# Kernel optimization log

Measured on AMD Instinct MI355X. Metric: run time of the kernel, lower is better.

Reference implementation:

```python
import jax, jax.numpy as jnp
import numpy as np

MIN_NORM = 1e-15
BALL_EPS = 4e-3  # HGCN PoincareBall fp32 boundary eps
C = 1.0          # curvature (init kwarg c)
CLAMP = 1e6      # torch.clamp bound in HypAgg.forward


def _artanh(x):
    # torch Artanh clamps input into open (-1, 1); use fp32-safe eps
    return jnp.arctanh(jnp.clip(x, -1.0 + 1e-7, 1.0 - 1e-7))


def _norm(x):
    return jnp.maximum(jnp.linalg.norm(x, axis=-1, keepdims=True), MIN_NORM)


def mobius_add(x, y, c):
    x2 = jnp.sum(x * x, axis=-1, keepdims=True)
    y2 = jnp.sum(y * y, axis=-1, keepdims=True)
    xy = jnp.sum(x * y, axis=-1, keepdims=True)
    num = (1.0 + 2.0 * c * xy + c * y2) * x + (1.0 - c * x2) * y
    den = 1.0 + 2.0 * c * xy + (c * c) * x2 * y2
    return num / jnp.maximum(den, MIN_NORM)


def lambda_x(x, c):
    return 2.0 / jnp.maximum(1.0 - c * jnp.sum(x * x, axis=-1, keepdims=True), MIN_NORM)


def logmap(p1, p2, c):
    # log_{p1}(p2) on the Poincare ball
    sub = mobius_add(-p1, p2, c)
    sub_norm = _norm(sub)
    sqrt_c = c ** 0.5
    return (2.0 / sqrt_c / lambda_x(p1, c)) * _artanh(sqrt_c * sub_norm) * sub / sub_norm


def expmap(u, p, c):
    sqrt_c = c ** 0.5
    u_norm = _norm(u)
    second = jnp.tanh(sqrt_c / 2.0 * lambda_x(p, c) * u_norm) * u / (sqrt_c * u_norm)
    return mobius_add(p, second, c)


def proj(x, c):
    norm = _norm(x)
    maxnorm = (1.0 - BALL_EPS) / (c ** 0.5)
    return jnp.where(norm > maxnorm, x / norm * maxnorm, x)


def setup_inputs() -> dict:
    key = jax.random.key(0)
    kx, ka, kw = jax.random.split(key, 3)
    B, N, D = 2, 768, 64
    # points strictly inside the unit ball
    x = proj(0.2 * jax.random.normal(kx, (B, N, D), dtype=jnp.float32), C)
    adj = (jax.random.uniform(ka, (B, N, N), dtype=jnp.float32) < 0.05).astype(jnp.float32)
    att_W = jax.random.normal(kw, (2 * D, 1), dtype=jnp.float32) * (1.0 / np.sqrt(2 * D))
    att_b = jnp.zeros((1,), dtype=jnp.float32)
    return {"x": x, "adj": adj, "att_W": att_W, "att_b": att_b}


def reference(x, adj, att_W, att_b):
    c = C
    b, n, d = x.shape
    # pairwise tangent vectors: x_local[b,i,j] = log_{x_i}(x_j)   (b,n,n,d)
    x_i = x[:, :, None, :]
    x_j = x[:, None, :, :]
    x_local = logmap(x_i, x_j, c)
    # log_x(x) == 0 tangent, kept for faithfulness
    x_self = logmap(x, x, c)  # (b,n,d), ~0
    # DenseAtt: linear(2d->1) on [self_tangent || pairwise_tangent], sigmoid, masked by adj
    feats = jnp.concatenate(
        [jnp.broadcast_to(x_self[:, :, None, :], x_local.shape), x_local], axis=-1
    )  # (b,n,n,2d)
    logits = jnp.einsum('bijk,ko->bijo', feats, att_W)[..., 0] + att_b[0]  # (b,n,n)
    att = jax.nn.sigmoid(logits) * adj
    # attention-weighted tangent aggregation over neighbors j
    support_t = jnp.einsum('bij,bijd->bid', att, x_local)
    # proj_tan is identity on the Poincare ball
    support_t = jnp.clip(support_t, -CLAMP, CLAMP)
    return proj(expmap(support_t, x, c), c)
```

## Files before the change

### kernel.cpp

```cpp
#include <hip/hip_runtime.h>
#include <math.h>

#define NB 2
#define NN 768
#define ND 64
#define XSTRIDE 68

__device__ __forceinline__ float fmul_(float a, float b) { float r = a * b; asm volatile("" : "+v"(r)); return r; }
__device__ __forceinline__ float fadd_(float a, float b) { float r = a + b; asm volatile("" : "+v"(r)); return r; }

template <typename F>
__device__ __forceinline__ float pw64(F f) {
  float r[8];
#pragma unroll
  for (int m = 0; m < 8; ++m) r[m] = f(m);
#pragma unroll
  for (int i = 1; i < 8; ++i) {
#pragma unroll
    for (int m = 0; m < 8; ++m) r[m] = fadd_(r[m], f(8 * i + m));
  }
  const float s01 = fadd_(r[0], r[1]), s23 = fadd_(r[2], r[3]);
  const float s45 = fadd_(r[4], r[5]), s67 = fadd_(r[6], r[7]);
  return fadd_(fadd_(s01, s23), fadd_(s45, s67));
}

__device__ __forceinline__ float pwShfl(float v, int lane) {
  const int m = lane & 7;
  float s = __shfl(v, m);
#pragma unroll
  for (int i = 1; i < 8; ++i) s = fadd_(s, __shfl(v, m + 8 * i));
  s = fadd_(s, __shfl_xor(s, 1));
  s = fadd_(s, __shfl_xor(s, 2));
  s = fadd_(s, __shfl_xor(s, 4));
  return s;
}

__device__ __forceinline__ void pwShfl2(float va, float vb, int lane,
                                        float& sa, float& sb) {
  const int m = lane & 7;
  float a = __shfl(va, m), b = __shfl(vb, m);
#pragma unroll
  for (int i = 1; i < 8; ++i) {
    a = fadd_(a, __shfl(va, m + 8 * i));
    b = fadd_(b, __shfl(vb, m + 8 * i));
  }
  a = fadd_(a, __shfl_xor(a, 1)); b = fadd_(b, __shfl_xor(b, 1));
  a = fadd_(a, __shfl_xor(a, 2)); b = fadd_(b, __shfl_xor(b, 2));
  a = fadd_(a, __shfl_xor(a, 4)); b = fadd_(b, __shfl_xor(b, 4));
  sa = a; sb = b;
}

__device__ __forceinline__ float div_rn(float n, float d, float r) {
  const float q0 = n * r;
  const float e  = __builtin_fmaf(-d, q0, n);
  return __builtin_fmaf(e, r, q0);
}

__global__ __launch_bounds__(64) void k_main(const float* __restrict__ x,
                                             const float* __restrict__ adj,
                                             const float* __restrict__ attW,
                                             const float* __restrict__ attb,
                                             float* __restrict__ out) {
  __shared__ float xi_s[ND];
  __shared__ float sW2[ND];
  __shared__ short lj[NN];
  __shared__ float lds_x[64 * XSTRIDE];

  const int row  = blockIdx.x;
  const int b    = row / NN;
  const int lane = threadIdx.x;

  const float xiv = x[(size_t)row * ND + lane];
  xi_s[lane] = xiv;
  sW2[lane]  = attW[ND + lane];

  const float* __restrict__ arow = adj + (size_t)row * NN;
  float av[NN / 64];
#pragma unroll
  for (int c = 0; c < NN / 64; ++c) av[c] = arow[c * 64 + lane];

  const float ni = pwShfl(fmul_(xiv, xiv), lane);

  const float b1  = 1.0f - ni;
  const float lam = 2.0f / fmaxf(b1, 1e-15f);
  const float g1  = 2.0f / lam;
  const float ab  = attb[0];
  const float ATH_CLIP = (float)(1.0 - 1e-07);

  int count = 0, qb1 = 0, qb2 = 0, qb3 = 0;
#pragma unroll
  for (int c = 0; c < NN / 64; ++c) {
    const unsigned long long m = __ballot(av[c] != 0.0f);
    if (av[c] != 0.0f) {
      const int rank = __popcll(m & ((1ull << lane) - 1ull));
      lj[count + rank] = (short)(c * 64 + lane);
    }
    count += __popcll(m);
    if (c == 2) qb1 = count;
    if (c == 5) qb2 = count;
    if (c == 8) qb3 = count;
  }
  __syncthreads();

  const float* __restrict__ xb = x + (size_t)b * NN * ND;
  float pP = 0.0f;
  float Q0 = 0.0f, Q1 = 0.0f, Q2 = 0.0f, Q3 = 0.0f;
  float cfv = 0.0f;

  for (int base = 0; base < count; base += 64) {
    const int valid = min(count - base, 64);

    if (lane < valid) {
      const int j = lj[base + lane];
      float rj[ND];
      const float4* __restrict__ xj4 = (const float4*)(xb + (size_t)j * ND);
#pragma unroll
      for (int k4 = 0; k4 < 16; ++k4) {
        const float4 v = xj4[k4];
        rj[4 * k4 + 0] = v.x; rj[4 * k4 + 1] = v.y;
        rj[4 * k4 + 2] = v.z; rj[4 * k4 + 3] = v.w;
      }
      {
        float4* __restrict__ dst = (float4*)&lds_x[lane * XSTRIDE];
#pragma unroll
        for (int k4 = 0; k4 < 16; ++k4)
          dst[k4] = make_float4(rj[4 * k4], rj[4 * k4 + 1],
                                rj[4 * k4 + 2], rj[4 * k4 + 3]);
      }
      const float nj = pw64([&](int k) { return fmul_(rj[k], rj[k]); });
      const float d  = pw64([&](int k) { return fmul_(xi_s[k], rj[k]); });
      const float xy = -d;
      const float t1  = fadd_(1.0f, 2.0f * xy);
      const float a1  = fadd_(t1, nj);
      const float den = fadd_(t1, fmul_(ni, nj));
      const float denc = fmaxf(den, 1e-15f);
      const float rden = 1.0f / denc;
      float racc[8];
      float subW = 0.0f;
#pragma unroll
      for (int m = 0; m < 8; ++m) {
        const float nk = fadd_(-fmul_(a1, xi_s[m]), fmul_(b1, rj[m]));
        const float sk = div_rn(nk, denc, rden);
        subW = __builtin_fmaf(sk, sW2[m], subW);
        racc[m] = fmul_(sk, sk);
      }
#pragma unroll
      for (int i8 = 1; i8 < 8; ++i8) {
#pragma unroll
        for (int m = 0; m < 8; ++m) {
          const int k = 8 * i8 + m;
          const float nk = fadd_(-fmul_(a1, xi_s[k]), fmul_(b1, rj[k]));
          const float sk = div_rn(nk, denc, rden);
          subW = __builtin_fmaf(sk, sW2[k], subW);
          racc[m] = fadd_(racc[m], fmul_(sk, sk));
        }
      }
      const float s01 = fadd_(racc[0], racc[1]), s23 = fadd_(racc[2], racc[3]);
      const float s45 = fadd_(racc[4], racc[5]), s67 = fadd_(racc[6], racc[7]);
      const float s2  = fadd_(fadd_(s01, s23), fadd_(s45, s67));
      const float t   = sqrtf(s2);
      const float sn  = fmaxf(t, 1e-15f);
      const float z   = fminf(sn, ATH_CLIP);
      const float ath = atanhf(z);
      const float g2  = fmul_(g1, ath);
      const float gg  = g2 / sn;
      const float logit = gg * subW + ab;
      const float sig   = 1.0f / (1.0f + expf(-logit));
      const float cfac  = sig * gg * rden;
      cfv = cfac;
      pP = __builtin_fmaf(cfac, a1, pP);
    }
    __syncthreads();

    const int lim = base + valid;
    {
      const int lo = max(0,   base), hi = min(qb1, lim);
      for (int p2 = lo; p2 < hi; ++p2)
        Q0 = __builtin_fmaf(__shfl(cfv, p2 - base),
                            lds_x[(p2 - base) * XSTRIDE + lane], Q0);
    }
    {
      const int lo = max(qb1, base), hi = min(qb2, lim);
      for (int p2 = lo; p2 < hi; ++p2)
        Q1 = __builtin_fmaf(__shfl(cfv, p2 - base),
                            lds_x[(p2 - base) * XSTRIDE + lane], Q1);
    }
    {
      const int lo = max(qb2, base), hi = min(qb3, lim);
      for (int p2 = lo; p2 < hi; ++p2)
        Q2 = __builtin_fmaf(__shfl(cfv, p2 - base),
                            lds_x[(p2 - base) * XSTRIDE + lane], Q2);
    }
    {
      const int lo = max(qb3, base), hi = min(count, lim);
      for (int p2 = lo; p2 < hi; ++p2)
        Q3 = __builtin_fmaf(__shfl(cfv, p2 - base),
                            lds_x[(p2 - base) * XSTRIDE + lane], Q3);
    }
    __syncthreads();
  }

  float pw = pP;
#pragma unroll
  for (int m = 32; m >= 1; m >>= 1) pw += __shfl_xor(pw, m, 64);
  const float P = pw;
  const float Q = (Q0 + Q1) + (Q2 + Q3);

  float u = b1 * Q - P * xiv;
  u = fminf(fmaxf(u, -1e6f), 1e6f);
  const float u2 = pwShfl(fmul_(u, u), lane);
  const float un = fmaxf(sqrtf(u2), 1e-15f);
  const float th = tanhf(fmul_(0.5f * lam, un));
  const float sec = fmul_(th, u) / un;
  float y2, xys;
  pwShfl2(fmul_(sec, sec), fmul_(xiv, sec), lane, y2, xys);
  const float t1e  = fadd_(1.0f, 2.0f * xys);
  const float a1e  = fadd_(t1e, y2);
  const float dene = fmaxf(fadd_(t1e, fmul_(ni, y2)), 1e-15f);
  const float o    = fadd_(fmul_(a1e, xiv), fmul_(b1, sec)) / dene;
  const float o2 = pwShfl(fmul_(o, o), lane);
  const float nm = fmaxf(sqrtf(o2), 1e-15f);
  const float res = (nm > 0.996f) ? fmul_(o / nm, 0.996f) : o;
  out[(size_t)row * ND + lane] = res;
}

extern "C" void kernel_launch(void* const* d_in, const int* in_sizes, int n_in,
                              void* d_out, int out_size, void* d_ws, size_t ws_size,
                              hipStream_t stream) {
  const float* x    = (const float*)d_in[0];
  const float* adj  = (const float*)d_in[1];
  const float* attW = (const float*)d_in[2];
  const float* attb = (const float*)d_in[3];
  float* out = (float*)d_out;

  hipLaunchKernelGGL(k_main, dim3(NB * NN), dim3(64), 0, stream,
                     x, adj, attW, attb, out);
}
```

Baseline: 74.18 us.

## Split neighbor list across two wavefronts per row with per-wave LDS buffers

Measured after the change: 83.86 us. 13.0% more time.

```diff
diff --git a/kernel.cpp b/kernel.cpp
--- a/kernel.cpp
+++ b/kernel.cpp
@@ -5,6 +5,7 @@
 #define NN 768
 #define ND 64
 #define XSTRIDE 68
+#define CH 32
 
 __device__ __forceinline__ float fmul_(float a, float b) { float r = a * b; asm volatile("" : "+v"(r)); return r; }
 __device__ __forceinline__ float fadd_(float a, float b) { float r = a + b; asm volatile("" : "+v"(r)); return r; }
@@ -56,19 +57,24 @@
   return __builtin_fmaf(e, r, q0);
 }
 
-__global__ __launch_bounds__(64) void k_main(const float* __restrict__ x,
-                                             const float* __restrict__ adj,
-                                             const float* __restrict__ attW,
-                                             const float* __restrict__ attb,
-                                             float* __restrict__ out) {
+__global__ __launch_bounds__(128, 3) void k_main(const float* __restrict__ x,
+                                                 const float* __restrict__ adj,
+                                                 const float* __restrict__ attW,
+                                                 const float* __restrict__ attb,
+                                                 float* __restrict__ out) {
   __shared__ float xi_s[ND];
   __shared__ float sW2[ND];
   __shared__ short lj[NN];
-  __shared__ float lds_x[64 * XSTRIDE];
+  __shared__ float cf_s[2][CH];
+  __shared__ float lds_x[2][CH * XSTRIDE];
+  __shared__ float qbuf[ND];
+  __shared__ float pbuf[ND];
 
   const int row  = blockIdx.x;
   const int b    = row / NN;
-  const int lane = threadIdx.x;
+  const int tid  = threadIdx.x;
+  const int wv   = tid >> 6;
+  const int lane = tid & 63;
 
   const float xiv = x[(size_t)row * ND + lane];
   xi_s[lane] = xiv;
@@ -100,15 +106,17 @@
     if (c == 5) qb2 = count;
     if (c == 8) qb3 = count;
   }
-  __syncthreads();
 
   const float* __restrict__ xb = x + (size_t)b * NN * ND;
+  const int myLo = wv ? qb2 : 0;
+  const int myHi = wv ? count : qb2;
+  const int qMid = wv ? qb3 : qb1;
+
   float pP = 0.0f;
-  float Q0 = 0.0f, Q1 = 0.0f, Q2 = 0.0f, Q3 = 0.0f;
-  float cfv = 0.0f;
-
-  for (int base = 0; base < count; base += 64) {
-    const int valid = min(count - base, 64);
+  float Qa = 0.0f, Qb = 0.0f;
+
+  for (int base = myLo; base < myHi; base += CH) {
+    const int valid = min(myHi - base, CH);
 
     if (lane < valid) {
       const int j = lj[base + lane];
@@ -121,7 +129,7 @@
         rj[4 * k4 + 2] = v.z; rj[4 * k4 + 3] = v.w;
       }
       {
-        float4* __restrict__ dst = (float4*)&lds_x[lane * XSTRIDE];
+        float4* __restrict__ dst = (float4*)&lds_x[wv][lane * XSTRIDE];
 #pragma unroll
         for (int k4 = 0; k4 < 16; ++k4)
           dst[k4] = make_float4(rj[4 * k4], rj[4 * k4 + 1],
@@ -167,61 +175,73 @@
       const float logit = gg * subW + ab;
       const float sig   = 1.0f / (1.0f + expf(-logit));
       const float cfac  = sig * gg * rden;
-      cfv = cfac;
+      cf_s[wv][lane] = cfac;
       pP = __builtin_fmaf(cfac, a1, pP);
     }
-    __syncthreads();
 
     const int lim = base + valid;
     {
-      const int lo = max(0,   base), hi = min(qb1, lim);
-      for (int p2 = lo; p2 < hi; ++p2)
-        Q0 = __builtin_fmaf(__shfl(cfv, p2 - base),
-                            lds_x[(p2 - base) * XSTRIDE + lane], Q0);
+      const int lo = base, hi = min(qMid, lim);
+      int p = lo;
+      if (p < hi) {
+        float c0 = cf_s[wv][p - base];
+        float v0 = lds_x[wv][(p - base) * XSTRIDE + lane];
+        while (++p < hi) {
+          const float c1 = cf_s[wv][p - base];
+          const float v1 = lds_x[wv][(p - base) * XSTRIDE + lane];
+          Qa = __builtin_fmaf(c0, v0, Qa);
+          c0 = c1; v0 = v1;
+        }
+        Qa = __builtin_fmaf(c0, v0, Qa);
+      }
     }
     {
-      const int lo = max(qb1, base), hi = min(qb2, lim);
-      for (int p2 = lo; p2 < hi; ++p2)
-        Q1 = __builtin_fmaf(__shfl(cfv, p2 - base),
-                            lds_x[(p2 - base) * XSTRIDE + lane], Q1);
-    }
-    {
-      const int lo = max(qb2, base), hi = min(qb3, lim);
-      for (int p2 = lo; p2 < hi; ++p2)
-        Q2 = __builtin_fmaf(__shfl(cfv, p2 - base),
-                            lds_x[(p2 - base) * XSTRIDE + lane], Q2);
-    }
-    {
-      const int lo = max(qb3, base), hi = min(count, lim);
-      for (int p2 = lo; p2 < hi; ++p2)
-        Q3 = __builtin_fmaf(__shfl(cfv, p2 - base),
-                            lds_x[(p2 - base) * XSTRIDE + lane], Q3);
-    }
-    __syncthreads();
-  }
-
-  float pw = pP;
-#pragma unroll
-  for (int m = 32; m >= 1; m >>= 1) pw += __shfl_xor(pw, m, 64);
-  const float P = pw;
-  const float Q = (Q0 + Q1) + (Q2 + Q3);
-
-  float u = b1 * Q - P * xiv;
-  u = fminf(fmaxf(u, -1e6f), 1e6f);
-  const float u2 = pwShfl(fmul_(u, u), lane);
-  const float un = fmaxf(sqrtf(u2), 1e-15f);
-  const float th = tanhf(fmul_(0.5f * lam, un));
-  const float sec = fmul_(th, u) / un;
-  float y2, xys;
-  pwShfl2(fmul_(sec, sec), fmul_(xiv, sec), lane, y2, xys);
-  const float t1e  = fadd_(1.0f, 2.0f * xys);
-  const float a1e  = fadd_(t1e, y2);
-  const float dene = fmaxf(fadd_(t1e, fmul_(ni, y2)), 1e-15f);
-  const float o    = fadd_(fmul_(a1e, xiv), fmul_(b1, sec)) / dene;
-  const float o2 = pwShfl(fmul_(o, o), lane);
-  const float nm = fmaxf(sqrtf(o2), 1e-15f);
-  const float res = (nm > 0.996f) ? fmul_(o / nm, 0.996f) : o;
-  out[(size_t)row * ND + lane] = res;
+      const int lo = max(qMid, base), hi = lim;
+      int p = lo;
+      if (p < hi) {
+        float c0 = cf_s[wv][p - base];
+        float v0 = lds_x[wv][(p - base) * XSTRIDE + lane];
+        while (++p < hi) {
+          const float c1 = cf_s[wv][p - base];
+          const float v1 = lds_x[wv][(p - base) * XSTRIDE + lane];
+          Qb = __builtin_fmaf(c0, v0, Qb);
+          c0 = c1; v0 = v1;
+        }
+        Qb = __builtin_fmaf(c0, v0, Qb);
+      }
+    }
+  }
+
+  if (wv == 1) {
+    qbuf[lane] = fadd_(Qa, Qb);
+    pbuf[lane] = pP;
+  }
+  __syncthreads();
+  if (wv == 0) {
+    const float Q = fadd_(fadd_(Qa, Qb), qbuf[lane]);
+
+    float pw = pP + pbuf[lane];
+#pragma unroll
+    for (int m = 32; m >= 1; m >>= 1) pw += __shfl_xor(pw, m, 64);
+    const float P = pw;
+
+    float u = b1 * Q - P * xiv;
+    u = fminf(fmaxf(u, -1e6f), 1e6f);
+    const float u2 = pwShfl(fmul_(u, u), lane);
+    const float un = fmaxf(sqrtf(u2), 1e-15f);
+    const float th = tanhf(fmul_(0.5f * lam, un));
+    const float sec = fmul_(th, u) / un;
+    float y2, xys;
+    pwShfl2(fmul_(sec, sec), fmul_(xiv, sec), lane, y2, xys);
+    const float t1e  = fadd_(1.0f, 2.0f * xys);
+    const float a1e  = fadd_(t1e, y2);
+    const float dene = fmaxf(fadd_(t1e, fmul_(ni, y2)), 1e-15f);
+    const float o    = fadd_(fmul_(a1e, xiv), fmul_(b1, sec)) / dene;
+    const float o2 = pwShfl(fmul_(o, o), lane);
+    const float nm = fmaxf(sqrtf(o2), 1e-15f);
+    const float res = (nm > 0.996f) ? fmul_(o / nm, 0.996f) : o;
+    out[(size_t)row * ND + lane] = res;
+  }
 }
 
 extern "C" void kernel_launch(void* const* d_in, const int* in_sizes, int n_in,
@@ -233,6 +253,6 @@
   const float* attb = (const float*)d_in[3];
   float* out = (float*)d_out;
 
-  hipLaunchKernelGGL(k_main, dim3(NB * NN), dim3(64), 0, stream,
+  hipLaunchKernelGGL(k_main, dim3(NB * NN), dim3(128), 0, stream,
                      x, adj, attW, attb, out);
 }
```
